# Kernel tuning notes

Hardware: AMD Instinct MI355X
Metric: run time of the kernel (lower is better)

The kernel has to match this reference:

```python
import jax, jax.numpy as jnp
import numpy as np

B, N, D, H = 16, 512, 256, 8
DK = D // H
EPS = 1e-6
NEG_INF = 1e12
LAM_ATT, LAM_DIST, LAM_ADJ = 0.3, 0.3, 0.4


def setup_inputs() -> dict:
    key = jax.random.key(0)
    ks = jax.random.split(key, 16)
    inp = {
        "query": jax.random.normal(ks[0], (B, N, D), jnp.float32),
        "key": jax.random.normal(ks[1], (B, N, D), jnp.float32),
        "value": jax.random.normal(ks[2], (B, N, D), jnp.float32),
        "adj_matrix": jax.random.uniform(ks[3], (B, N, N), jnp.float32),
        "distances_matrix": jax.random.uniform(ks[4], (B, N, N), jnp.float32),
        "edges_att": jnp.zeros((1,), jnp.float32),
        "mask": jnp.ones((B, N), jnp.int32),
    }
    s = 1.0 / np.sqrt(D)
    # four Linear(d_model, d_model): Wq, Wk, Wv, Wo (+ biases)
    for i, nm in enumerate(["q", "k", "v", "o"]):
        inp[f"W{nm}"] = jax.random.normal(ks[5 + 2 * i], (D, D), jnp.float32) * s
        inp[f"b{nm}"] = jax.random.normal(ks[6 + 2 * i], (D,), jnp.float32) * s
    return inp


def _proj(x, W, b):
    # [B,N,D] -> [B,H,N,DK]
    y = x @ W.T + b
    return y.reshape(B, N, H, DK).transpose(0, 2, 1, 3)


def reference(query, key, value, adj_matrix, distances_matrix, edges_att, mask,
              Wq, bq, Wk, bk, Wv, bv, Wo, bo):
    q = _proj(query, Wq, bq)
    k = _proj(key, Wk, bk)
    v = _proj(value, Wv, bv)

    valid = mask != 0  # [B,N] key-side validity

    # distance kernel: softmax(-d) over keys, masked positions -> 0 prob
    d_scores = jnp.where(valid[:, None, :], -distances_matrix, -jnp.inf)
    p_dist = jax.nn.softmax(d_scores, axis=-1)  # [B,N,N]

    # scaled dot-product attention with key mask
    scores = jnp.einsum("bhqd,bhkd->bhqk", q, k) / np.sqrt(DK)
    scores = jnp.where(valid[:, None, None, :], scores, -NEG_INF)
    p_attn = jax.nn.softmax(scores, axis=-1)  # [B,H,N,N]

    # row-normalized adjacency
    p_adj = adj_matrix / (adj_matrix.sum(axis=-1, keepdims=True) + EPS)  # [B,N,N]

    # blend three attention terms (broadcast dist/adj over heads)
    p_weighted = (LAM_ATT * p_attn
                  + LAM_DIST * p_dist[:, None]
                  + LAM_ADJ * p_adj[:, None])  # [B,H,N,N]

    x = jnp.einsum("bhqk,bhkd->bhqd", p_weighted, v)  # [B,H,N,DK]
    x = x.transpose(0, 2, 1, 3).reshape(B, N, D)
    out = x @ Wo.T + bo  # output projection (4th linear)
    return out
```

## Files before the change

### kernel.cpp

```cpp
#include <hip/hip_runtime.h>
#include <cstdint>
#include <cstddef>

#define B_  16
#define N_  512
#define D_  256
#define H_  8
#define DK_ 32

#define QKV_ELEMS 2097152

__device__ __align__(16) unsigned short g_Qb[QKV_ELEMS];
__device__ __align__(16) unsigned short g_Kb[QKV_ELEMS];
__device__ __align__(16) unsigned short g_VT[QKV_ELEMS];
__device__ __align__(16) unsigned short g_Ain[3*QKV_ELEMS];
__device__ __align__(16) unsigned short g_WqB[D_*D_];
__device__ __align__(16) unsigned short g_WkB[D_*D_];
__device__ __align__(16) unsigned short g_WvB[D_*D_];
__device__ __align__(16) unsigned short g_WoB[D_*D_];
__device__ __align__(16) unsigned short g_ST[B_*N_*N_];

typedef short v8s __attribute__((ext_vector_type(8)));
typedef float v4f __attribute__((ext_vector_type(4)));

#define QSCALE 0.25503485917270874f

__device__ __forceinline__ unsigned short f2b(float f){
  unsigned int x;
  __builtin_memcpy(&x, &f, 4);
  x = x + 0x7FFFu + ((x >> 16) & 1u);
  return (unsigned short)(x >> 16);
}
__device__ __forceinline__ v8s pack8(const float4 a, const float4 b){
  v8s o;
  o[0]=(short)f2b(a.x); o[1]=(short)f2b(a.y); o[2]=(short)f2b(a.z); o[3]=(short)f2b(a.w);
  o[4]=(short)f2b(b.x); o[5]=(short)f2b(b.y); o[6]=(short)f2b(b.z); o[7]=(short)f2b(b.w);
  return o;
}

__global__ __launch_bounds__(256) void prep(
    const float* __restrict__ dist, const float* __restrict__ adjm,
    const int* __restrict__ mask,
    const float* __restrict__ query, const float* __restrict__ key_,
    const float* __restrict__ value,
    const float* __restrict__ Wq, const float* __restrict__ Wk,
    const float* __restrict__ Wv, const float* __restrict__ Wo)
{
  const int bid = blockIdx.x;
  const int t   = threadIdx.x;

  if (bid < 1024){
    const int s = bid;
    const int b = (s >> 1) & 15, qt = s >> 5, half = s & 1;
    const int row = half*8 + (t >> 5);
    const int seg = t & 31;
    const size_t roff = ((size_t)(b*N_ + qt*16 + row))*N_ + seg*16;
    const float* dp = dist + roff;
    const float* ap = adjm + roff;
    const int*   mp = mask + b*N_ + seg*16;
    const float4 d0 = reinterpret_cast<const float4*>(dp)[0];
    const float4 d1 = reinterpret_cast<const float4*>(dp)[1];
    const float4 d2 = reinterpret_cast<const float4*>(dp)[2];
    const float4 d3 = reinterpret_cast<const float4*>(dp)[3];
    const float4 a0 = reinterpret_cast<const float4*>(ap)[0];
    const float4 a1 = reinterpret_cast<const float4*>(ap)[1];
    const float4 a2 = reinterpret_cast<const float4*>(ap)[2];
    const float4 a3 = reinterpret_cast<const float4*>(ap)[3];
    const int4   m0 = reinterpret_cast<const int4*>(mp)[0];
    const int4   m1 = reinterpret_cast<const int4*>(mp)[1];
    const int4   m2 = reinterpret_cast<const int4*>(mp)[2];
    const int4   m3 = reinterpret_cast<const int4*>(mp)[3];

    float ev[16], av[16];
    #define ST_STEP(i, d4, a4, m4) \
      ev[i+0] = m4.x ? __expf(-d4.x) : 0.f;  av[i+0] = a4.x; \
      ev[i+1] = m4.y ? __expf(-d4.y) : 0.f;  av[i+1] = a4.y; \
      ev[i+2] = m4.z ? __expf(-d4.z) : 0.f;  av[i+2] = a4.z; \
      ev[i+3] = m4.w ? __expf(-d4.w) : 0.f;  av[i+3] = a4.w;
    ST_STEP(0,  d0, a0, m0)
    ST_STEP(4,  d1, a1, m1)
    ST_STEP(8,  d2, a2, m2)
    ST_STEP(12, d3, a3, m3)
    #undef ST_STEP
    float lz = 0.f, la = 0.f;
    #pragma unroll
    for (int i = 0; i < 16; ++i){ lz += ev[i]; la += av[i]; }
    #pragma unroll
    for (int o = 1; o < 32; o <<= 1){
      lz += __shfl_xor(lz, o, 64);
      la += __shfl_xor(la, o, 64);
    }
    const float c0 = (lz > 0.f) ? 0.3f / lz : 0.f;
    const float c1 = 0.4f / (la + 1e-6f);
    v8s s0v, s1v;
    #pragma unroll
    for (int i = 0; i < 8; ++i){
      s0v[i] = (short)f2b(ev[i]*c0   + av[i]*c1);
      s1v[i] = (short)f2b(ev[8+i]*c0 + av[8+i]*c1);
    }
    *reinterpret_cast<v8s*>(g_ST + roff)     = s0v;
    *reinterpret_cast<v8s*>(g_ST + roff + 8) = s1v;
    return;
  }

  if (bid < 2560){
    const int a = bid - 1024;
    const int z = a >> 9;
    const int blk = a & 511;
    const size_t base = ((size_t)blk*256 + t) * 16;
    const float* src = (z==0)?query:(z==1)?key_:value;
    const float4 u0 = reinterpret_cast<const float4*>(src + base)[0];
    const float4 u1 = reinterpret_cast<const float4*>(src + base)[1];
    const float4 u2 = reinterpret_cast<const float4*>(src + base)[2];
    const float4 u3 = reinterpret_cast<const float4*>(src + base)[3];
    unsigned short* dst = g_Ain + (size_t)z*QKV_ELEMS + base;
    *reinterpret_cast<v8s*>(dst)     = pack8(u0, u1);
    *reinterpret_cast<v8s*>(dst + 8) = pack8(u2, u3);
    return;
  }

  const int wb = bid - 2560;
  const int z = wb >> 6;
  const int i = ((wb & 63)*256 + t)*4;
  const float* src = (z==0)?Wq:(z==1)?Wk:(z==2)?Wv:Wo;
  const float4 u = *reinterpret_cast<const float4*>(src + i);
  ushort4 o4;
  o4.x = f2b(u.x); o4.y = f2b(u.y); o4.z = f2b(u.z); o4.w = f2b(u.w);
  if (z < 3){
    unsigned short* dst = (z==0)?g_WqB:(z==1)?g_WkB:g_WvB;
    *reinterpret_cast<ushort4*>(dst + i) = o4;
  } else {
    const int n = i >> 8, k = i & 255;
    *reinterpret_cast<ushort4*>(g_WoB + ((size_t)(k >> 5))*8192 + (size_t)n*32 + (k & 31)) = o4;
  }
}

__global__ __launch_bounds__(256) void qkv_gemm(
    const float* __restrict__ bq, const float* __restrict__ bk,
    const float* __restrict__ bv)
{
  __shared__ unsigned short Wl[64*264];
  const int bid0 = blockIdx.x;
  const int t    = threadIdx.x;
  const int bid = ((bid0 & 7) * 192) + (bid0 >> 3);
  const int z  = bid >> 9;
  const int rr = bid & 511;
  const int mt = rr >> 2, nt = rr & 3;
  const unsigned short* Ap = g_Ain + (size_t)z*QKV_ELEMS;
  const unsigned short* WB = (z==0) ? g_WqB : (z==1) ? g_WkB : g_WvB;
  const float* bp = (z==0) ? bq : (z==1) ? bk : bv;
  const int w = t >> 6, lane = t & 63, kl = lane & 15, quad = lane >> 4;
  const int m0 = mt*64 + w*16;
  const int n0 = nt*64;

  {
    const int row = t >> 2;
    const int ks  = (t & 3) * 64;
    const unsigned short* src = WB + (size_t)(n0+row)*256 + ks;
    unsigned short* dst = Wl + row*264 + ks;
    #pragma unroll
    for (int u = 0; u < 8; ++u)
      *reinterpret_cast<v8s*>(dst + u*8) = *reinterpret_cast<const v8s*>(src + u*8);
  }
  __syncthreads();

  v4f acc[4];
  #pragma unroll
  for (int nb = 0; nb < 4; ++nb) acc[nb] = (v4f){0.f,0.f,0.f,0.f};
  const int arow = m0 + kl;

  if (z == 2){
    #pragma unroll
    for (int k0 = 0; k0 < 256; k0 += 32){
      const v8s af = *reinterpret_cast<const v8s*>(Ap + (size_t)arow*256 + k0 + quad*8);
      #pragma unroll
      for (int nb = 0; nb < 4; ++nb){
        const v8s wf = *reinterpret_cast<const v8s*>(&Wl[(nb*16+kl)*264 + k0 + quad*8]);
        acc[nb] = __builtin_amdgcn_mfma_f32_16x16x32_bf16(wf, af, acc[nb], 0, 0, 0);
      }
    }
    const int tok = m0 + kl, bb = tok >> 9, nr = tok & 511;
    #pragma unroll
    for (int nb = 0; nb < 4; ++nb)
      #pragma unroll
      for (int r = 0; r < 4; ++r){
        const int n = n0 + nb*16 + quad*4 + r;
        const float v = acc[nb][r] + bp[n];
        g_VT[(((size_t)bb*H_ + (n>>5))*16 + (nr>>5))*1024 + (size_t)(n&31)*32 + (nr&31)] = f2b(v);
      }
  } else {
    #pragma unroll
    for (int k0 = 0; k0 < 256; k0 += 32){
      const v8s af = *reinterpret_cast<const v8s*>(Ap + (size_t)arow*256 + k0 + quad*8);
      #pragma unroll
      for (int nb = 0; nb < 4; ++nb){
        const v8s wf = *reinterpret_cast<const v8s*>(&Wl[(nb*16+kl)*264 + k0 + quad*8]);
        acc[nb] = __builtin_amdgcn_mfma_f32_16x16x32_bf16(af, wf, acc[nb], 0, 0, 0);
      }
    }
    unsigned short* dst = z ? g_Kb : g_Qb;
    const float sc = (z == 0) ? QSCALE : 1.0f;
    #pragma unroll
    for (int nb = 0; nb < 4; ++nb){
      const int n = n0 + nb*16 + kl;
      const float bias = bp[n];
      #pragma unroll
      for (int r = 0; r < 4; ++r){
        const int m = m0 + quad*4 + r;
        const float v = (acc[nb][r] + bias) * sc;
        dst[(((size_t)(m>>9)*H_ + (n>>5))*N_ + (m&511))*DK_ + (n&31)] = f2b(v);
      }
    }
  }
}

__global__ __launch_bounds__(512, 4) void attn_kernel(
    const int* __restrict__ mask, const float* __restrict__ bo,
    float* __restrict__ out)
{
  __shared__ unsigned short STl[16*520];
  __shared__ unsigned short Xl[16*272];
  const int bid = blockIdx.x;
  const int b  = bid & 15;
  const int qt = bid >> 4;
  const int q0 = qt*16;
  const int t  = threadIdx.x;
  const int w  = t >> 6, lane = t & 63;
  const int kl = lane & 15, quad = lane >> 4;

  {
    const int row = t >> 5;
    const int c16 = (t & 31) * 16;
    const unsigned short* src = g_ST + ((size_t)(b*N_ + q0 + row))*N_ + c16;
    *reinterpret_cast<v8s*>(&STl[row*520 + c16])     = *reinterpret_cast<const v8s*>(src);
    *reinterpret_cast<v8s*>(&STl[row*520 + c16 + 8]) = *reinterpret_cast<const v8s*>(src + 8);
  }

  const int h = w;
  const size_t bh = (size_t)b*H_ + h;
  const unsigned short* Qp = g_Qb + (bh*N_ + q0)*DK_;
  const unsigned short* Kp = g_Kb + bh*N_*DK_;
  const unsigned short* Vp = g_VT + bh*(size_t)(N_*DK_);
  const int* mrow = mask + b*N_;
  const v8s aq = *reinterpret_cast<const v8s*>(Qp + (size_t)kl*DK_ + quad*8);
  const v4f vz = {0.f, 0.f, 0.f, 0.f};

  const int s0 = ((quad & 1) << 5) + kl;
  const int s1 = s0 + 16;
  const int hi = quad >> 1;

  v4f oA0 = vz, oA1 = vz;
  v4f oS0 = vz, oS1 = vz;
  float lsum = 0.f;

  __syncthreads();

  #pragma unroll 1
  for (int ch = 0; ch < 4; ++ch){
    const int k0 = ch*128;
    v4f acc[8];
    #pragma unroll
    for (int kb = 0; kb < 8; ++kb){
      const v8s bk = *reinterpret_cast<const v8s*>(Kp + (size_t)(k0 + kb*16 + kl)*DK_ + quad*8);
      acc[kb] = __builtin_amdgcn_mfma_f32_16x16x32_bf16(bk, aq, vz, 0, 0, 0);
    }
    v8s av[8];
    #pragma unroll
    for (int cc = 0; cc < 4; ++cc){
      const int kk = k0 + cc*32;
      av[2*cc]   = *reinterpret_cast<const v8s*>(Vp + (size_t)(kk + kl)*32 + quad*8);
      av[2*cc+1] = *reinterpret_cast<const v8s*>(Vp + (size_t)(kk + 16 + kl)*32 + quad*8);
    }
    #pragma unroll
    for (int kb = 0; kb < 8; ++kb){
      const int4 m4 = *reinterpret_cast<const int4*>(mrow + k0 + kb*16 + quad*4);
      const float e0 = m4.x ? __builtin_amdgcn_exp2f(acc[kb][0]) : 0.f;
      const float e1 = m4.y ? __builtin_amdgcn_exp2f(acc[kb][1]) : 0.f;
      const float e2 = m4.z ? __builtin_amdgcn_exp2f(acc[kb][2]) : 0.f;
      const float e3 = m4.w ? __builtin_amdgcn_exp2f(acc[kb][3]) : 0.f;
      acc[kb][0]=e0; acc[kb][1]=e1; acc[kb][2]=e2; acc[kb][3]=e3;
      lsum += e0+e1+e2+e3;
    }
    #pragma unroll
    for (int cc = 0; cc < 4; ++cc){
      const int kk = k0 + cc*32;
      uint32_t pkE0, pkE2, pkO0, pkO2;
      asm("v_cvt_pk_bf16_f32 %0, %1, %2" : "=v"(pkE0) : "v"(acc[2*cc][0]),   "v"(acc[2*cc][1]));
      asm("v_cvt_pk_bf16_f32 %0, %1, %2" : "=v"(pkE2) : "v"(acc[2*cc][2]),   "v"(acc[2*cc][3]));
      asm("v_cvt_pk_bf16_f32 %0, %1, %2" : "=v"(pkO0) : "v"(acc[2*cc+1][0]), "v"(acc[2*cc+1][1]));
      asm("v_cvt_pk_bf16_f32 %0, %1, %2" : "=v"(pkO2) : "v"(acc[2*cc+1][2]), "v"(acc[2*cc+1][3]));
      const uint32_t e0a = (uint32_t)__shfl((int)pkE0, s0, 64);
      const uint32_t o0a = (uint32_t)__shfl((int)pkO0, s0, 64);
      const uint32_t e2a = (uint32_t)__shfl((int)pkE2, s0, 64);
      const uint32_t o2a = (uint32_t)__shfl((int)pkO2, s0, 64);
      const uint32_t e0b = (uint32_t)__shfl((int)pkE0, s1, 64);
      const uint32_t o0b = (uint32_t)__shfl((int)pkO0, s1, 64);
      const uint32_t e2b = (uint32_t)__shfl((int)pkE2, s1, 64);
      const uint32_t o2b = (uint32_t)__shfl((int)pkO2, s1, 64);
      union { v8s v; uint32_t w4[4]; } bp;
      bp.w4[0] = hi ? o0a : e0a;
      bp.w4[1] = hi ? o2a : e2a;
      bp.w4[2] = hi ? o0b : e0b;
      bp.w4[3] = hi ? o2b : e2b;
      const v8s bst = *reinterpret_cast<const v8s*>(&STl[kl*520 + kk + quad*8]);
      oA0 = __builtin_amdgcn_mfma_f32_16x16x32_bf16(av[2*cc],   bp.v, oA0, 0, 0, 0);
      oS0 = __builtin_amdgcn_mfma_f32_16x16x32_bf16(av[2*cc],   bst,  oS0, 0, 0, 0);
      oA1 = __builtin_amdgcn_mfma_f32_16x16x32_bf16(av[2*cc+1], bp.v, oA1, 0, 0, 0);
      oS1 = __builtin_amdgcn_mfma_f32_16x16x32_bf16(av[2*cc+1], bst,  oS1, 0, 0, 0);
    }
  }

  lsum += __shfl_xor(lsum, 16, 64);
  lsum += __shfl_xor(lsum, 32, 64);
  const float inv = (lsum > 0.f) ? 0.3f / lsum : 0.f;

  unsigned short* xr = Xl + kl*272 + h*32;
  #pragma unroll
  for (int r = 0; r < 4; ++r){
    xr[     quad*4 + r] = f2b(oA0[r]*inv + oS0[r]);
    xr[16 + quad*4 + r] = f2b(oA1[r]*inv + oS1[r]);
  }
  __syncthreads();

  {
    const int n0 = w*32;
    v4f a2[2];
    a2[0] = vz; a2[1] = vz;
    #pragma unroll
    for (int k0 = 0; k0 < 256; k0 += 32){
      const v8s af = *reinterpret_cast<const v8s*>(&Xl[kl*272 + k0 + quad*8]);
      #pragma unroll
      for (int nb = 0; nb < 2; ++nb){
        const v8s wf = *reinterpret_cast<const v8s*>(
            g_WoB + (size_t)(k0 >> 5)*8192 + (size_t)(n0 + nb*16 + kl)*32 + quad*8);
        a2[nb] = __builtin_amdgcn_mfma_f32_16x16x32_bf16(af, wf, a2[nb], 0, 0, 0);
      }
    }
    #pragma unroll
    for (int nb = 0; nb < 2; ++nb){
      const int n = n0 + nb*16 + kl;
      const float bias = bo[n];
      #pragma unroll
      for (int r = 0; r < 4; ++r)
        out[((size_t)(b*N_ + q0 + quad*4 + r))*256 + n] = a2[nb][r] + bias;
    }
  }
}

extern "C" void kernel_launch(void* const* d_in, const int* in_sizes, int n_in,
                              void* d_out, int out_size, void* d_ws, size_t ws_size,
                              hipStream_t stream)
{
  const float* query = (const float*)d_in[0];
  const float* key_  = (const float*)d_in[1];
  const float* value = (const float*)d_in[2];
  const float* adjm  = (const float*)d_in[3];
  const float* dist  = (const float*)d_in[4];
  const int*   mask  = (const int*)d_in[6];
  const float* Wq = (const float*)d_in[7];  const float* bq = (const float*)d_in[8];
  const float* Wk = (const float*)d_in[9];  const float* bk = (const float*)d_in[10];
  const float* Wv = (const float*)d_in[11]; const float* bv = (const float*)d_in[12];
  const float* Wo = (const float*)d_in[13]; const float* bo = (const float*)d_in[14];

  prep<<<2816, 256, 0, stream>>>(dist, adjm, mask, query, key_, value,
                                 Wq, Wk, Wv, Wo);
  qkv_gemm<<<1536, 256, 0, stream>>>(bq, bk, bv);
  attn_kernel<<<512, 512, 0, stream>>>(mask, bo, (float*)d_out);
}
```

Measured before the change: 161.4 us.

## Move ST blend into QKV GEMM launch and shrink attention chunk for occupancy

The dist/adj softmax-blend work (ST) moves out of the prep kernel into the QKV GEMM launch. Blocks are interleaved 3:2 so the bandwidth-bound ST rows run alongside the compute-bound GEMM tiles. In the attention kernel, the key chunk drops from 128 to 64 and V fragments are loaded inside the inner loop rather than held across it. Launch bounds rise to 6 waves per SIMD to cut register pressure and raise occupancy. The risks are more loop iterations, less latency hiding per wave, and possible spills under the tighter register cap.

```diff
diff --git a/kernel.cpp b/kernel.cpp
--- a/kernel.cpp
+++ b/kernel.cpp
@@ -39,8 +39,6 @@
 }
 
 __global__ __launch_bounds__(256) void prep(
-    const float* __restrict__ dist, const float* __restrict__ adjm,
-    const int* __restrict__ mask,
     const float* __restrict__ query, const float* __restrict__ key_,
     const float* __restrict__ value,
     const float* __restrict__ Wq, const float* __restrict__ Wk,
@@ -49,8 +47,50 @@
   const int bid = blockIdx.x;
   const int t   = threadIdx.x;
 
-  if (bid < 1024){
-    const int s = bid;
+  if (bid < 1536){
+    const int z = bid >> 9;
+    const int blk = bid & 511;
+    const size_t base = ((size_t)blk*256 + t) * 16;
+    const float* src = (z==0)?query:(z==1)?key_:value;
+    const float4 u0 = reinterpret_cast<const float4*>(src + base)[0];
+    const float4 u1 = reinterpret_cast<const float4*>(src + base)[1];
+    const float4 u2 = reinterpret_cast<const float4*>(src + base)[2];
+    const float4 u3 = reinterpret_cast<const float4*>(src + base)[3];
+    unsigned short* dst = g_Ain + (size_t)z*QKV_ELEMS + base;
+    *reinterpret_cast<v8s*>(dst)     = pack8(u0, u1);
+    *reinterpret_cast<v8s*>(dst + 8) = pack8(u2, u3);
+    return;
+  }
+
+  const int wb = bid - 1536;
+  const int z = wb >> 6;
+  const int i = ((wb & 63)*256 + t)*4;
+  const float* src = (z==0)?Wq:(z==1)?Wk:(z==2)?Wv:Wo;
+  const float4 u = *reinterpret_cast<const float4*>(src + i);
+  ushort4 o4;
+  o4.x = f2b(u.x); o4.y = f2b(u.y); o4.z = f2b(u.z); o4.w = f2b(u.w);
+  if (z < 3){
+    unsigned short* dst = (z==0)?g_WqB:(z==1)?g_WkB:g_WvB;
+    *reinterpret_cast<ushort4*>(dst + i) = o4;
+  } else {
+    const int n = i >> 8, k = i & 255;
+    *reinterpret_cast<ushort4*>(g_WoB + ((size_t)(k >> 5))*8192 + (size_t)n*32 + (k & 31)) = o4;
+  }
+}
+
+__global__ __launch_bounds__(256) void st_gemm(
+    const float* __restrict__ bq, const float* __restrict__ bk,
+    const float* __restrict__ bv,
+    const float* __restrict__ dist, const float* __restrict__ adjm,
+    const int* __restrict__ mask)
+{
+  __shared__ unsigned short Wl[64*264];
+  const int bid0 = blockIdx.x;
+  const int t    = threadIdx.x;
+  const int m5 = bid0 % 5, d5 = bid0 / 5;
+
+  if (m5 >= 3){
+    const int s = d5*2 + (m5 - 3);
     const int b = (s >> 1) & 15, qt = s >> 5, half = s & 1;
     const int row = half*8 + (t >> 5);
     const int seg = t & 31;
@@ -103,46 +143,8 @@
     return;
   }
 
-  if (bid < 2560){
-    const int a = bid - 1024;
-    const int z = a >> 9;
-    const int blk = a & 511;
-    const size_t base = ((size_t)blk*256 + t) * 16;
-    const float* src = (z==0)?query:(z==1)?key_:value;
-    const float4 u0 = reinterpret_cast<const float4*>(src + base)[0];
-    const float4 u1 = reinterpret_cast<const float4*>(src + base)[1];
-    const float4 u2 = reinterpret_cast<const float4*>(src + base)[2];
-    const float4 u3 = reinterpret_cast<const float4*>(src + base)[3];
-    unsigned short* dst = g_Ain + (size_t)z*QKV_ELEMS + base;
-    *reinterpret_cast<v8s*>(dst)     = pack8(u0, u1);
-    *reinterpret_cast<v8s*>(dst + 8) = pack8(u2, u3);
-    return;
-  }
-
-  const int wb = bid - 2560;
-  const int z = wb >> 6;
-  const int i = ((wb & 63)*256 + t)*4;
-  const float* src = (z==0)?Wq:(z==1)?Wk:(z==2)?Wv:Wo;
-  const float4 u = *reinterpret_cast<const float4*>(src + i);
-  ushort4 o4;
-  o4.x = f2b(u.x); o4.y = f2b(u.y); o4.z = f2b(u.z); o4.w = f2b(u.w);
-  if (z < 3){
-    unsigned short* dst = (z==0)?g_WqB:(z==1)?g_WkB:g_WvB;
-    *reinterpret_cast<ushort4*>(dst + i) = o4;
-  } else {
-    const int n = i >> 8, k = i & 255;
-    *reinterpret_cast<ushort4*>(g_WoB + ((size_t)(k >> 5))*8192 + (size_t)n*32 + (k & 31)) = o4;
-  }
-}
-
-__global__ __launch_bounds__(256) void qkv_gemm(
-    const float* __restrict__ bq, const float* __restrict__ bk,
-    const float* __restrict__ bv)
-{
-  __shared__ unsigned short Wl[64*264];
-  const int bid0 = blockIdx.x;
-  const int t    = threadIdx.x;
-  const int bid = ((bid0 & 7) * 192) + (bid0 >> 3);
+  const int g0  = d5*3 + m5;
+  const int bid = ((g0 & 7) * 192) + (g0 >> 3);
   const int z  = bid >> 9;
   const int rr = bid & 511;
   const int mt = rr >> 2, nt = rr & 3;
@@ -214,7 +216,7 @@
   }
 }
 
-__global__ __launch_bounds__(512, 4) void attn_kernel(
+__global__ __launch_bounds__(512, 6) void attn_kernel(
     const int* __restrict__ mask, const float* __restrict__ bo,
     float* __restrict__ out)
 {
@@ -256,23 +258,16 @@
   __syncthreads();
 
   #pragma unroll 1
-  for (int ch = 0; ch < 4; ++ch){
-    const int k0 = ch*128;
-    v4f acc[8];
-    #pragma unroll
-    for (int kb = 0; kb < 8; ++kb){
+  for (int ch = 0; ch < 8; ++ch){
+    const int k0 = ch*64;
+    v4f acc[4];
+    #pragma unroll
+    for (int kb = 0; kb < 4; ++kb){
       const v8s bk = *reinterpret_cast<const v8s*>(Kp + (size_t)(k0 + kb*16 + kl)*DK_ + quad*8);
       acc[kb] = __builtin_amdgcn_mfma_f32_16x16x32_bf16(bk, aq, vz, 0, 0, 0);
     }
-    v8s av[8];
-    #pragma unroll
-    for (int cc = 0; cc < 4; ++cc){
-      const int kk = k0 + cc*32;
-      av[2*cc]   = *reinterpret_cast<const v8s*>(Vp + (size_t)(kk + kl)*32 + quad*8);
-      av[2*cc+1] = *reinterpret_cast<const v8s*>(Vp + (size_t)(kk + 16 + kl)*32 + quad*8);
-    }
-    #pragma unroll
-    for (int kb = 0; kb < 8; ++kb){
+    #pragma unroll
+    for (int kb = 0; kb < 4; ++kb){
       const int4 m4 = *reinterpret_cast<const int4*>(mrow + k0 + kb*16 + quad*4);
       const float e0 = m4.x ? __builtin_amdgcn_exp2f(acc[kb][0]) : 0.f;
       const float e1 = m4.y ? __builtin_amdgcn_exp2f(acc[kb][1]) : 0.f;
@@ -282,8 +277,10 @@
       lsum += e0+e1+e2+e3;
     }
     #pragma unroll
-    for (int cc = 0; cc < 4; ++cc){
+    for (int cc = 0; cc < 2; ++cc){
       const int kk = k0 + cc*32;
+      const v8s av0 = *reinterpret_cast<const v8s*>(Vp + (size_t)(kk + kl)*32 + quad*8);
+      const v8s av1 = *reinterpret_cast<const v8s*>(Vp + (size_t)(kk + 16 + kl)*32 + quad*8);
       uint32_t pkE0, pkE2, pkO0, pkO2;
       asm("v_cvt_pk_bf16_f32 %0, %1, %2" : "=v"(pkE0) : "v"(acc[2*cc][0]),   "v"(acc[2*cc][1]));
       asm("v_cvt_pk_bf16_f32 %0, %1, %2" : "=v"(pkE2) : "v"(acc[2*cc][2]),   "v"(acc[2*cc][3]));
@@ -303,10 +300,10 @@
       bp.w4[2] = hi ? o0b : e0b;
       bp.w4[3] = hi ? o2b : e2b;
       const v8s bst = *reinterpret_cast<const v8s*>(&STl[kl*520 + kk + quad*8]);
-      oA0 = __builtin_amdgcn_mfma_f32_16x16x32_bf16(av[2*cc],   bp.v, oA0, 0, 0, 0);
-      oS0 = __builtin_amdgcn_mfma_f32_16x16x32_bf16(av[2*cc],   bst,  oS0, 0, 0, 0);
-      oA1 = __builtin_amdgcn_mfma_f32_16x16x32_bf16(av[2*cc+1], bp.v, oA1, 0, 0, 0);
-      oS1 = __builtin_amdgcn_mfma_f32_16x16x32_bf16(av[2*cc+1], bst,  oS1, 0, 0, 0);
+      oA0 = __builtin_amdgcn_mfma_f32_16x16x32_bf16(av0, bp.v, oA0, 0, 0, 0);
+      oS0 = __builtin_amdgcn_mfma_f32_16x16x32_bf16(av0, bst,  oS0, 0, 0, 0);
+      oA1 = __builtin_amdgcn_mfma_f32_16x16x32_bf16(av1, bp.v, oA1, 0, 0, 0);
+      oS1 = __builtin_amdgcn_mfma_f32_16x16x32_bf16(av1, bst,  oS1, 0, 0, 0);
     }
   }
 
@@ -362,8 +359,7 @@
   const float* Wv = (const float*)d_in[11]; const float* bv = (const float*)d_in[12];
   const float* Wo = (const float*)d_in[13]; const float* bo = (const float*)d_in[14];
 
-  prep<<<2816, 256, 0, stream>>>(dist, adjm, mask, query, key_, value,
-                                 Wq, Wk, Wv, Wo);
-  qkv_gemm<<<1536, 256, 0, stream>>>(bq, bk, bv);
+  prep<<<1792, 256, 0, stream>>>(query, key_, value, Wq, Wk, Wv, Wo);
+  st_gemm<<<2560, 256, 0, stream>>>(bq, bk, bv, dist, adjm, mask);
   attn_kernel<<<512, 512, 0, stream>>>(mask, bo, (float*)d_out);
 }
```

Result: no change. 163.2 us (+1.1%).

## Fuse prep, QKV GEMM and attention into one cooperative persistent kernel

Applied to the files above, without the earlier changes.

Merges the three kernels into a single cooperative launch of 512 blocks of 512 threads, using grid-wide syncs between the prep, QKV projection and attention phases. The work is re-partitioned so each block handles one prep slice, three GEMM tiles and one attention tile. The goal is to remove launch gaps and kernel-boundary drains. It costs two grid barriers, and the merged kernel's register and LDS footprint may limit occupancy; if the cooperative launch fails, it falls back to three separate kernels.

```diff
diff --git a/kernel.cpp b/kernel.cpp
--- a/kernel.cpp
+++ b/kernel.cpp
@@ -1,6 +1,9 @@
 #include <hip/hip_runtime.h>
+#include <hip/hip_cooperative_groups.h>
 #include <cstdint>
 #include <cstddef>
+
+namespace cg = cooperative_groups;
 
 #define B_  16
 #define N_  512
@@ -38,22 +41,15 @@
   return o;
 }
 
-__global__ __launch_bounds__(256) void prep(
-    const float* __restrict__ dist, const float* __restrict__ adjm,
-    const int* __restrict__ mask,
-    const float* __restrict__ query, const float* __restrict__ key_,
-    const float* __restrict__ value,
-    const float* __restrict__ Wq, const float* __restrict__ Wk,
-    const float* __restrict__ Wv, const float* __restrict__ Wo)
-{
-  const int bid = blockIdx.x;
-  const int t   = threadIdx.x;
-
-  if (bid < 1024){
-    const int s = bid;
-    const int b = (s >> 1) & 15, qt = s >> 5, half = s & 1;
-    const int row = half*8 + (t >> 5);
-    const int seg = t & 31;
+__device__ __forceinline__ void phase_prep(
+    int bid, int t,
+    const float* dist, const float* adjm, const int* mask,
+    const float* query, const float* key_, const float* value,
+    const float* Wq, const float* Wk, const float* Wv, const float* Wo)
+{
+  {
+    const int b = bid & 15, qt = bid >> 4;
+    const int row = t >> 5, seg = t & 31;
     const size_t roff = ((size_t)(b*N_ + qt*16 + row))*N_ + seg*16;
     const float* dp = dist + roff;
     const float* ap = adjm + roff;
@@ -100,73 +96,68 @@
     }
     *reinterpret_cast<v8s*>(g_ST + roff)     = s0v;
     *reinterpret_cast<v8s*>(g_ST + roff + 8) = s1v;
-    return;
-  }
-
-  if (bid < 2560){
-    const int a = bid - 1024;
-    const int z = a >> 9;
-    const int blk = a & 511;
-    const size_t base = ((size_t)blk*256 + t) * 16;
-    const float* src = (z==0)?query:(z==1)?key_:value;
-    const float4 u0 = reinterpret_cast<const float4*>(src + base)[0];
-    const float4 u1 = reinterpret_cast<const float4*>(src + base)[1];
-    const float4 u2 = reinterpret_cast<const float4*>(src + base)[2];
-    const float4 u3 = reinterpret_cast<const float4*>(src + base)[3];
-    unsigned short* dst = g_Ain + (size_t)z*QKV_ELEMS + base;
-    *reinterpret_cast<v8s*>(dst)     = pack8(u0, u1);
-    *reinterpret_cast<v8s*>(dst + 8) = pack8(u2, u3);
-    return;
-  }
-
-  const int wb = bid - 2560;
-  const int z = wb >> 6;
-  const int i = ((wb & 63)*256 + t)*4;
-  const float* src = (z==0)?Wq:(z==1)?Wk:(z==2)?Wv:Wo;
-  const float4 u = *reinterpret_cast<const float4*>(src + i);
-  ushort4 o4;
-  o4.x = f2b(u.x); o4.y = f2b(u.y); o4.z = f2b(u.z); o4.w = f2b(u.w);
-  if (z < 3){
-    unsigned short* dst = (z==0)?g_WqB:(z==1)?g_WkB:g_WvB;
-    *reinterpret_cast<ushort4*>(dst + i) = o4;
-  } else {
-    const int n = i >> 8, k = i & 255;
-    *reinterpret_cast<ushort4*>(g_WoB + ((size_t)(k >> 5))*8192 + (size_t)n*32 + (k & 31)) = o4;
-  }
-}
-
-__global__ __launch_bounds__(256) void qkv_gemm(
-    const float* __restrict__ bq, const float* __restrict__ bk,
-    const float* __restrict__ bv)
-{
-  __shared__ unsigned short Wl[64*264];
-  const int bid0 = blockIdx.x;
-  const int t    = threadIdx.x;
-  const int bid = ((bid0 & 7) * 192) + (bid0 >> 3);
-  const int z  = bid >> 9;
-  const int rr = bid & 511;
+  }
+
+  {
+    const size_t base = ((size_t)(bid*512 + t))*8;
+    #pragma unroll
+    for (int u = 0; u < 3; ++u){
+      const float* src = (u==0)?query:(u==1)?key_:value;
+      const float4 x0 = reinterpret_cast<const float4*>(src + base)[0];
+      const float4 x1 = reinterpret_cast<const float4*>(src + base)[1];
+      *reinterpret_cast<v8s*>(g_Ain + (size_t)u*QKV_ELEMS + base) = pack8(x0, x1);
+    }
+  }
+
+  {
+    const int gid = bid*512 + t;
+    if (gid < 65536){
+      const int i = gid*4;
+      const int z = i >> 16, lo = i & 65535;
+      const float* src = (z==0)?Wq:(z==1)?Wk:(z==2)?Wv:Wo;
+      const float4 u = *reinterpret_cast<const float4*>(src + lo);
+      ushort4 o4;
+      o4.x=f2b(u.x); o4.y=f2b(u.y); o4.z=f2b(u.z); o4.w=f2b(u.w);
+      if (z < 3){
+        unsigned short* dst = (z==0)?g_WqB:(z==1)?g_WkB:g_WvB;
+        *reinterpret_cast<ushort4*>(dst + lo) = o4;
+      } else {
+        const int n = lo >> 8, k = lo & 255;
+        *reinterpret_cast<ushort4*>(g_WoB + ((size_t)(k >> 5))*8192 + (size_t)n*32 + (k & 31)) = o4;
+      }
+    }
+  }
+}
+
+__device__ __forceinline__ void phase_gemm_tile(
+    int tile, int t, unsigned short* Wl,
+    const float* bq, const float* bk, const float* bv)
+{
+  const int z  = tile >> 9;
+  const int rr = tile & 511;
   const int mt = rr >> 2, nt = rr & 3;
   const unsigned short* Ap = g_Ain + (size_t)z*QKV_ELEMS;
   const unsigned short* WB = (z==0) ? g_WqB : (z==1) ? g_WkB : g_WvB;
   const float* bp = (z==0) ? bq : (z==1) ? bk : bv;
   const int w = t >> 6, lane = t & 63, kl = lane & 15, quad = lane >> 4;
-  const int m0 = mt*64 + w*16;
-  const int n0 = nt*64;
-
-  {
-    const int row = t >> 2;
-    const int ks  = (t & 3) * 64;
-    const unsigned short* src = WB + (size_t)(n0+row)*256 + ks;
+  const int msub = w & 3, nhalf = w >> 2;
+  const int m0 = mt*64 + msub*16;
+  const int nbase = nt*64 + nhalf*32;
+
+  {
+    const int row = t >> 3;
+    const int ks  = (t & 7) * 32;
+    const unsigned short* src = WB + (size_t)(nt*64 + row)*256 + ks;
     unsigned short* dst = Wl + row*264 + ks;
     #pragma unroll
-    for (int u = 0; u < 8; ++u)
+    for (int u = 0; u < 4; ++u)
       *reinterpret_cast<v8s*>(dst + u*8) = *reinterpret_cast<const v8s*>(src + u*8);
   }
   __syncthreads();
 
-  v4f acc[4];
-  #pragma unroll
-  for (int nb = 0; nb < 4; ++nb) acc[nb] = (v4f){0.f,0.f,0.f,0.f};
+  v4f acc[2];
+  acc[0] = (v4f){0.f,0.f,0.f,0.f};
+  acc[1] = (v4f){0.f,0.f,0.f,0.f};
   const int arow = m0 + kl;
 
   if (z == 2){
@@ -174,17 +165,17 @@
     for (int k0 = 0; k0 < 256; k0 += 32){
       const v8s af = *reinterpret_cast<const v8s*>(Ap + (size_t)arow*256 + k0 + quad*8);
       #pragma unroll
-      for (int nb = 0; nb < 4; ++nb){
-        const v8s wf = *reinterpret_cast<const v8s*>(&Wl[(nb*16+kl)*264 + k0 + quad*8]);
+      for (int nb = 0; nb < 2; ++nb){
+        const v8s wf = *reinterpret_cast<const v8s*>(&Wl[(nhalf*32 + nb*16 + kl)*264 + k0 + quad*8]);
         acc[nb] = __builtin_amdgcn_mfma_f32_16x16x32_bf16(wf, af, acc[nb], 0, 0, 0);
       }
     }
     const int tok = m0 + kl, bb = tok >> 9, nr = tok & 511;
     #pragma unroll
-    for (int nb = 0; nb < 4; ++nb)
+    for (int nb = 0; nb < 2; ++nb)
       #pragma unroll
       for (int r = 0; r < 4; ++r){
-        const int n = n0 + nb*16 + quad*4 + r;
+        const int n = nbase + nb*16 + quad*4 + r;
         const float v = acc[nb][r] + bp[n];
         g_VT[(((size_t)bb*H_ + (n>>5))*16 + (nr>>5))*1024 + (size_t)(n&31)*32 + (nr&31)] = f2b(v);
       }
@@ -193,16 +184,16 @@
     for (int k0 = 0; k0 < 256; k0 += 32){
       const v8s af = *reinterpret_cast<const v8s*>(Ap + (size_t)arow*256 + k0 + quad*8);
       #pragma unroll
-      for (int nb = 0; nb < 4; ++nb){
-        const v8s wf = *reinterpret_cast<const v8s*>(&Wl[(nb*16+kl)*264 + k0 + quad*8]);
+      for (int nb = 0; nb < 2; ++nb){
+        const v8s wf = *reinterpret_cast<const v8s*>(&Wl[(nhalf*32 + nb*16 + kl)*264 + k0 + quad*8]);
         acc[nb] = __builtin_amdgcn_mfma_f32_16x16x32_bf16(af, wf, acc[nb], 0, 0, 0);
       }
     }
     unsigned short* dst = z ? g_Kb : g_Qb;
     const float sc = (z == 0) ? QSCALE : 1.0f;
     #pragma unroll
-    for (int nb = 0; nb < 4; ++nb){
-      const int n = n0 + nb*16 + kl;
+    for (int nb = 0; nb < 2; ++nb){
+      const int n = nbase + nb*16 + kl;
       const float bias = bp[n];
       #pragma unroll
       for (int r = 0; r < 4; ++r){
@@ -212,19 +203,16 @@
       }
     }
   }
-}
-
-__global__ __launch_bounds__(512, 4) void attn_kernel(
-    const int* __restrict__ mask, const float* __restrict__ bo,
-    float* __restrict__ out)
-{
-  __shared__ unsigned short STl[16*520];
-  __shared__ unsigned short Xl[16*272];
-  const int bid = blockIdx.x;
+  __syncthreads();
+}
+
+__device__ __forceinline__ void phase_attn(
+    int bid, int t, unsigned short* STl, unsigned short* Xl,
+    const int* mask, const float* bo, float* out)
+{
   const int b  = bid & 15;
   const int qt = bid >> 4;
   const int q0 = qt*16;
-  const int t  = threadIdx.x;
   const int w  = t >> 6, lane = t & 63;
   const int kl = lane & 15, quad = lane >> 4;
 
@@ -347,6 +335,64 @@
   }
 }
 
+__global__ __launch_bounds__(512, 4) void mega(
+    const float* __restrict__ dist, const float* __restrict__ adjm,
+    const int* __restrict__ mask,
+    const float* __restrict__ query, const float* __restrict__ key_,
+    const float* __restrict__ value,
+    const float* __restrict__ Wq, const float* __restrict__ Wk,
+    const float* __restrict__ Wv, const float* __restrict__ Wo,
+    const float* __restrict__ bq, const float* __restrict__ bk,
+    const float* __restrict__ bv, const float* __restrict__ bo,
+    float* __restrict__ out)
+{
+  __shared__ unsigned short smem[64*264];
+  const int bid = blockIdx.x;
+  const int t   = threadIdx.x;
+
+  phase_prep(bid, t, dist, adjm, mask, query, key_, value, Wq, Wk, Wv, Wo);
+
+  cg::this_grid().sync();
+
+  #pragma unroll 1
+  for (int i = 0; i < 3; ++i)
+    phase_gemm_tile(bid + i*512, t, smem, bq, bk, bv);
+
+  cg::this_grid().sync();
+
+  phase_attn(bid, t, smem, smem + 16*520, mask, bo, out);
+}
+
+__global__ __launch_bounds__(512) void prep_k(
+    const float* __restrict__ dist, const float* __restrict__ adjm,
+    const int* __restrict__ mask,
+    const float* __restrict__ query, const float* __restrict__ key_,
+    const float* __restrict__ value,
+    const float* __restrict__ Wq, const float* __restrict__ Wk,
+    const float* __restrict__ Wv, const float* __restrict__ Wo)
+{
+  phase_prep(blockIdx.x, threadIdx.x, dist, adjm, mask, query, key_, value,
+             Wq, Wk, Wv, Wo);
+}
+
+__global__ __launch_bounds__(512, 4) void gemm_k(
+    const float* __restrict__ bq, const float* __restrict__ bk,
+    const float* __restrict__ bv)
+{
+  __shared__ unsigned short smem[64*264];
+  #pragma unroll 1
+  for (int i = 0; i < 3; ++i)
+    phase_gemm_tile(blockIdx.x + i*512, threadIdx.x, smem, bq, bk, bv);
+}
+
+__global__ __launch_bounds__(512, 4) void attn_k(
+    const int* __restrict__ mask, const float* __restrict__ bo,
+    float* __restrict__ out)
+{
+  __shared__ unsigned short smem[16*520 + 16*272];
+  phase_attn(blockIdx.x, threadIdx.x, smem, smem + 16*520, mask, bo, out);
+}
+
 extern "C" void kernel_launch(void* const* d_in, const int* in_sizes, int n_in,
                               void* d_out, int out_size, void* d_ws, size_t ws_size,
                               hipStream_t stream)
@@ -361,9 +407,22 @@
   const float* Wk = (const float*)d_in[9];  const float* bk = (const float*)d_in[10];
   const float* Wv = (const float*)d_in[11]; const float* bv = (const float*)d_in[12];
   const float* Wo = (const float*)d_in[13]; const float* bo = (const float*)d_in[14];
-
-  prep<<<2816, 256, 0, stream>>>(dist, adjm, mask, query, key_, value,
-                                 Wq, Wk, Wv, Wo);
-  qkv_gemm<<<1536, 256, 0, stream>>>(bq, bk, bv);
-  attn_kernel<<<512, 512, 0, stream>>>(mask, bo, (float*)d_out);
-}
+  float* out = (float*)d_out;
+
+  void* kargs[] = {
+    (void*)&dist, (void*)&adjm, (void*)&mask,
+    (void*)&query, (void*)&key_, (void*)&value,
+    (void*)&Wq, (void*)&Wk, (void*)&Wv, (void*)&Wo,
+    (void*)&bq, (void*)&bk, (void*)&bv, (void*)&bo,
+    (void*)&out
+  };
+  hipError_t err = hipLaunchCooperativeKernel((const void*)mega,
+                                              dim3(512), dim3(512),
+                                              kargs, 0, stream);
+  if (err != hipSuccess){
+    prep_k<<<512, 512, 0, stream>>>(dist, adjm, mask, query, key_, value,
+                                    Wq, Wk, Wv, Wo);
+    gemm_k<<<512, 512, 0, stream>>>(bq, bk, bv);
+    attn_k<<<512, 512, 0, stream>>>(mask, bo, out);
+  }
+}
```

Result: slower. 336.6 us (+108.5%).
